# Performance work log

Hardware: AMD Instinct MI355X
Metric: run time of the kernel (lower is better)

The kernel has to match this reference:

```python
import jax, jax.numpy as jnp
import numpy as np

B_, L, DM = 2, 2048, 1024
DI, N, K, R = 2048, 16, 4, 64  # d_inner, d_state, d_conv, dt_rank


def setup_inputs() -> dict:
    key = jax.random.key(0)
    ks = jax.random.split(key, 8)
    return {
        "x": jax.random.normal(ks[0], (B_, L, DM), jnp.float32),
        "W_in": jax.random.normal(ks[1], (DM, 2 * DI), jnp.float32) * 0.02,
        "w_conv": jax.random.normal(ks[2], (DI, K), jnp.float32) * 0.1,
        "b_conv": jnp.zeros((DI,), jnp.float32),
        "W_x": jax.random.normal(ks[3], (DI, R + 2 * N), jnp.float32) * 0.02,
        "W_dt": jax.random.normal(ks[4], (R, DI), jnp.float32) * 0.02,
        "b_dt": jnp.full((DI,), -4.6, jnp.float32),  # softplus(b_dt) ~ 0.01 dt init
        "A_log": jnp.log(jnp.broadcast_to(jnp.arange(1, N + 1, dtype=jnp.float32), (DI, N))),
        "D": jnp.ones((DI,), jnp.float32),
        "W_out": jax.random.normal(ks[5], (DI, DM), jnp.float32) * 0.02,
        "gamma": jnp.ones((DM,), jnp.float32),
        "beta": jnp.zeros((DM,), jnp.float32),
    }


def reference(x, W_in, w_conv, b_conv, W_x, W_dt, b_dt, A_log, D, W_out, gamma, beta):
    Bb, Ll, Dm = x.shape
    Di, Kk = w_conv.shape
    Nn = A_log.shape[1]
    Rr = W_dt.shape[0]
    # in_proj -> (u, z)
    xz = x @ W_in  # [B,L,2*Di]
    u, z = jnp.split(xz, 2, axis=-1)
    # depthwise causal conv1d (kernel K, left pad K-1) + SiLU
    up = jnp.pad(u, ((0, 0), (Kk - 1, 0), (0, 0)))
    conv = b_conv + sum(up[:, k:k + Ll, :] * w_conv[:, k] for k in range(Kk))
    u = jax.nn.silu(conv)  # [B,L,Di]
    # x_proj -> dt, B, C
    dbc = u @ W_x
    dt, Bm, Cm = dbc[..., :Rr], dbc[..., Rr:Rr + Nn], dbc[..., Rr + Nn:]
    delta = jax.nn.softplus(dt @ W_dt + b_dt)  # [B,L,Di]
    A = -jnp.exp(A_log)  # [Di,N]

    def step(h, inputs):
        d_t, B_t, C_t, u_t = inputs  # [B,Di],[B,N],[B,N],[B,Di]
        dA = jnp.exp(d_t[..., None] * A)            # [B,Di,N]
        h = h * dA + (d_t * u_t)[..., None] * B_t[:, None, :]
        y = jnp.einsum('bdn,bn->bd', h, C_t)
        return h, y

    h0 = jnp.zeros((Bb, Di, Nn), x.dtype)
    _, ys = jax.lax.scan(step, h0, (delta.transpose(1, 0, 2), Bm.transpose(1, 0, 2),
                                    Cm.transpose(1, 0, 2), u.transpose(1, 0, 2)))
    y = ys.transpose(1, 0, 2)        # [B,L,Di]
    y = y + u * D                    # skip term
    y = y * jax.nn.silu(z)           # gate
    out = y @ W_out                  # [B,L,Dm]
    # LayerNorm
    mu = out.mean(-1, keepdims=True)
    var = ((out - mu) ** 2).mean(-1, keepdims=True)
    out = (out - mu) * jax.lax.rsqrt(var + 1e-5) * gamma + beta
    # dropout p=0 -> identity; residual
    return out + x
```

## Files before the change

### kernel.cpp

```cpp
#include <hip/hip_runtime.h>
#include <math.h>

#define L_SEQ 2048
#define DMOD  1024
#define DIN   2048
#define NBATCH 2
#define NTOK  (NBATCH * L_SEQ)
#define NST   16
#define RRANK 64
#define LOG2E 1.44269504088896f

#define GCHUNK 128
#define CLEN   (L_SEQ / GCHUNK)
#define SCHUNK 8
#define NSTAGE (CLEN / SCHUNK)

#define G4_KS   4
#define G4_KC   (2048 / G4_KS)
#define G2_KS   16
#define G2_KC   (2048 / G2_KS)

typedef __attribute__((ext_vector_type(8))) short  short8;
typedef __attribute__((ext_vector_type(4))) float  f32x4;

__device__ __forceinline__ ushort f2bf(float f) {
    unsigned u = __float_as_uint(f);
    u += 0x7fffu + ((u >> 16) & 1u);
    return (ushort)(u >> 16);
}
__device__ __forceinline__ float bf2f(ushort u) {
    return __uint_as_float(((unsigned)u) << 16);
}
__device__ __forceinline__ float fexp2(float x) {
    return __builtin_amdgcn_exp2f(x);
}

__device__ __forceinline__ void gload16(const ushort* g, ushort* l) {
    __builtin_amdgcn_global_load_lds(
        (const __attribute__((address_space(1))) unsigned int*)g,
        (__attribute__((address_space(3))) unsigned int*)l,
        16, 0, 0);
}

__device__ __forceinline__ void cast_body(
    const float* __restrict__ src, ushort* __restrict__ dst, int bid, int tid)
{
    int i = (bid * 256 + tid) * 8;
    float4 a = *(const float4*)(src + i);
    float4 b = *(const float4*)(src + i + 4);
    ushort4 o0 = make_ushort4(f2bf(a.x), f2bf(a.y), f2bf(a.z), f2bf(a.w));
    ushort4 o1 = make_ushort4(f2bf(b.x), f2bf(b.y), f2bf(b.z), f2bf(b.w));
    *(ushort4*)(dst + i)     = o0;
    *(ushort4*)(dst + i + 4) = o1;
}

__device__ __forceinline__ void tcast_body(
    const float* __restrict__ src, ushort* __restrict__ dst,
    int R, int C, int bx, int by, int tid)
{
    __shared__ float t[32][33];
    int tx = tid & 31;
    int ty = tid >> 5;
    int c0 = bx * 32;
    int r0 = by * 32;
    #pragma unroll
    for (int i = 0; i < 4; ++i)
        t[ty + i * 8][tx] = src[(size_t)(r0 + ty + i * 8) * C + c0 + tx];
    __syncthreads();
    #pragma unroll
    for (int i = 0; i < 4; ++i)
        dst[(size_t)(c0 + ty + i * 8) * R + r0 + tx] = f2bf(t[tx][ty + i * 8]);
}

__global__ __launch_bounds__(256) void prep_k(
    const float* __restrict__ x, const float* __restrict__ W_in,
    const float* __restrict__ W_dt, const float* __restrict__ W_x,
    const float* __restrict__ W_out,
    ushort* __restrict__ xb, ushort* __restrict__ Wib,
    ushort* __restrict__ Wdtb, ushort* __restrict__ Wxb,
    ushort* __restrict__ Wob)
{
    int bid = blockIdx.x, tid = threadIdx.x;
    if (bid < 2048) {
        cast_body(x, xb, bid, tid);
    } else if (bid < 6144) {
        int t = bid - 2048;
        tcast_body(W_in, Wib, 1024, 4096, t & 127, t >> 7, tid);
    } else if (bid < 6272) {
        int t = bid - 6144;
        tcast_body(W_dt, Wdtb, 64, 2048, t & 63, t >> 6, tid);
    } else if (bid < 6464) {
        int t = bid - 6272;
        tcast_body(W_x, Wxb, 2048, 96, t % 3, t / 3, tid);
    } else {
        int t = bid - 6464;
        tcast_body(W_out, Wob, 2048, 1024, t & 31, t >> 5, tid);
    }
}

__global__ __launch_bounds__(512, 2) void gemm8p(
    const ushort* __restrict__ A,
    const ushort* __restrict__ Bt,
    ushort* __restrict__ C,
    int K, int kslice, int ldc, size_t zstride,
    ushort* __restrict__ C2, int nsplit)
{
    __shared__ ushort lds[65536];

    const int tid  = threadIdx.x;
    const int wave = tid >> 6;
    const int lane = tid & 63;
    const int wr   = wave >> 2;
    const int wc   = wave & 3;

    const int gx = gridDim.x;
    int flat = blockIdx.y * gx + blockIdx.x;
    const int cpx = (gx * gridDim.y) >> 3;
    flat = (flat & 7) * cpx + (flat >> 3);
    const int bx = flat % gx;
    const int by = flat / gx;
    const int m0 = by * 256;
    const int n0 = bx * 256;
    const int kbeg = blockIdx.z * kslice;
    const int NT   = kslice >> 6;

    const int rr  = tid >> 2;
    const int gsw = ((tid & 3) ^ ((tid >> 3) & 3)) * 8;
    const ushort* a0 = A  + (size_t)(m0 + rr)        * K + kbeg + gsw;
    const ushort* a1 = A  + (size_t)(m0 + 128 + rr)  * K + kbeg + gsw;
    const ushort* b0 = Bt + (size_t)(n0 + rr)        * K + kbeg + gsw;
    const ushort* b1 = Bt + (size_t)(n0 + 128 + rr)  * K + kbeg + gsw;

    #define STAGE_U(op_, ks_, kt_, bf_) do {                                   \
        const int ko_ = (kt_) * 64 + (ks_) * 32;                               \
        ushort* l_ = lds + (bf_) * 32768 + (op_) * 16384 + (ks_) * 8192        \
                         + wave * 512;                                         \
        if ((op_) == 0) { gload16(a0 + ko_, l_); gload16(a1 + ko_, l_ + 4096); }\
        else            { gload16(b0 + ko_, l_); gload16(b1 + ko_, l_ + 4096); }\
    } while (0)

    const int lr  = lane & 15;
    const int swr = ((lane >> 4) ^ ((lr >> 1) & 3)) * 8;

    #define LDA(i_, ks_) (*(const short8*)&lds[buf * 32768 + (ks_) * 8192      \
        + (wr * 128 + (i_) * 16 + lr) * 32 + swr])
    #define LDB(j_, ks_) (*(const short8*)&lds[buf * 32768 + 16384             \
        + (ks_) * 8192 + (wc * 64 + (j_) * 16 + lr) * 32 + swr])

    f32x4 acc[8][4];
    #pragma unroll
    for (int i = 0; i < 8; ++i)
        #pragma unroll
        for (int j = 0; j < 4; ++j)
            acc[i][j] = (f32x4){0.f, 0.f, 0.f, 0.f};

    STAGE_U(0, 0, 0, 0); STAGE_U(1, 0, 0, 0);
    STAGE_U(0, 1, 0, 0); STAGE_U(1, 1, 0, 0);
    asm volatile("s_waitcnt vmcnt(4)" ::: "memory");
    __builtin_amdgcn_s_barrier();

    short8 a_[4], b_[4];

    for (int t = 0; t < NT; ++t) {
        const int buf = t & 1, nb = buf ^ 1;
        const bool st = (t + 1 < NT);

        #pragma unroll
        for (int i = 0; i < 4; ++i) a_[i] = LDA(i, 0);
        #pragma unroll
        for (int j = 0; j < 4; ++j) b_[j] = LDB(j, 0);
        if (st) STAGE_U(0, 0, t + 1, nb);
        __builtin_amdgcn_s_barrier();
        asm volatile("s_waitcnt lgkmcnt(0)" ::: "memory");
        __builtin_amdgcn_sched_barrier(0);
        __builtin_amdgcn_s_setprio(1);
        #pragma unroll
        for (int i = 0; i < 4; ++i)
            #pragma unroll
            for (int j = 0; j < 4; ++j)
                acc[i][j] = __builtin_amdgcn_mfma_f32_16x16x32_bf16(
                    a_[i], b_[j], acc[i][j], 0, 0, 0);
        __builtin_amdgcn_s_setprio(0);
        __builtin_amdgcn_s_barrier();

        #pragma unroll
        for (int i = 0; i < 4; ++i) a_[i] = LDA(4 + i, 0);
        if (st) {
            STAGE_U(1, 0, t + 1, nb);
            asm volatile("s_waitcnt vmcnt(4)" ::: "memory");
        } else {
            asm volatile("s_waitcnt vmcnt(0)" ::: "memory");
        }
        __builtin_amdgcn_s_barrier();
        asm volatile("s_waitcnt lgkmcnt(0)" ::: "memory");
        __builtin_amdgcn_sched_barrier(0);
        __builtin_amdgcn_s_setprio(1);
        #pragma unroll
        for (int i = 0; i < 4; ++i)
            #pragma unroll
            for (int j = 0; j < 4; ++j)
                acc[4 + i][j] = __builtin_amdgcn_mfma_f32_16x16x32_bf16(
                    a_[i], b_[j], acc[4 + i][j], 0, 0, 0);
        __builtin_amdgcn_s_setprio(0);
        __builtin_amdgcn_s_barrier();

        #pragma unroll
        for (int i = 0; i < 4; ++i) a_[i] = LDA(i, 1);
        #pragma unroll
        for (int j = 0; j < 4; ++j) b_[j] = LDB(j, 1);
        if (st) STAGE_U(0, 1, t + 1, nb);
        __builtin_amdgcn_s_barrier();
        asm volatile("s_waitcnt lgkmcnt(0)" ::: "memory");
        __builtin_amdgcn_sched_barrier(0);
        __builtin_amdgcn_s_setprio(1);
        #pragma unroll
        for (int i = 0; i < 4; ++i)
            #pragma unroll
            for (int j = 0; j < 4; ++j)
                acc[i][j] = __builtin_amdgcn_mfma_f32_16x16x32_bf16(
                    a_[i], b_[j], acc[i][j], 0, 0, 0);
        __builtin_amdgcn_s_setprio(0);
        __builtin_amdgcn_s_barrier();

        #pragma unroll
        for (int i = 0; i < 4; ++i) a_[i] = LDA(4 + i, 1);
        if (st) {
            STAGE_U(1, 1, t + 1, nb);
            asm volatile("s_waitcnt vmcnt(4)" ::: "memory");
        }
        __builtin_amdgcn_s_barrier();
        asm volatile("s_waitcnt lgkmcnt(0)" ::: "memory");
        __builtin_amdgcn_sched_barrier(0);
        __builtin_amdgcn_s_setprio(1);
        #pragma unroll
        for (int i = 0; i < 4; ++i)
            #pragma unroll
            for (int j = 0; j < 4; ++j)
                acc[4 + i][j] = __builtin_amdgcn_mfma_f32_16x16x32_bf16(
                    a_[i], b_[j], acc[4 + i][j], 0, 0, 0);
        __builtin_amdgcn_s_setprio(0);
        __builtin_amdgcn_s_barrier();
    }
    #undef STAGE_U
    #undef LDA
    #undef LDB

    ushort* Cp = C + (size_t)blockIdx.z * zstride;
    int ncol = n0;
    if (C2 != nullptr && n0 >= nsplit) { Cp = C2; ncol = n0 - nsplit; }
    const int rb = m0 + wr * 128 + ((lane >> 4) << 2);
    const int cb = ncol + wc * 64 + lr;
    #pragma unroll
    for (int i = 0; i < 8; ++i)
        #pragma unroll
        for (int j = 0; j < 4; ++j)
            #pragma unroll
            for (int r = 0; r < 4; ++r)
                Cp[(size_t)(rb + i * 16 + r) * ldc + cb + j * 16] =
                    f2bf(acc[i][j][r]);
}

template<int EPI, int OBF>
__global__ __launch_bounds__(256) void gemm_mfma(
    const ushort* __restrict__ A,
    const ushort* __restrict__ Bt,
    void* __restrict__ Cv,
    int M, int N, int K, int ldc, const float* __restrict__ bias)
{
    __shared__ ushort As[128 * 32];
    __shared__ ushort Bs[128 * 32];

    const int tid  = threadIdx.x;
    const int wave = tid >> 6;
    const int lane = tid & 63;
    const int wm   = (wave & 1) * 64;
    const int wn   = (wave >> 1) * 64;
    const int m0   = blockIdx.y * 128;
    const int n0   = blockIdx.x * 128;

    const int srow = lane >> 2;
    const int sg   = (lane & 3) ^ ((srow >> 1) & 3);
    const ushort* gA0 = A  + (size_t)(m0 + wave * 32 + srow)      * K + sg * 8;
    const ushort* gA1 = A  + (size_t)(m0 + wave * 32 + 16 + srow) * K + sg * 8;
    const ushort* gB0 = Bt + (size_t)(n0 + wave * 32 + srow)      * K + sg * 8;
    const ushort* gB1 = Bt + (size_t)(n0 + wave * 32 + 16 + srow) * K + sg * 8;
    ushort* lA0 = As + (wave * 32)      * 32;
    ushort* lA1 = As + (wave * 32 + 16) * 32;
    ushort* lB0 = Bs + (wave * 32)      * 32;
    ushort* lB1 = Bs + (wave * 32 + 16) * 32;

    const int lrow = lane & 15;
    const int swr  = ((lane >> 4) ^ ((lrow >> 1) & 3)) * 8;

    f32x4 acc[4][4];
    #pragma unroll
    for (int i = 0; i < 4; ++i)
        #pragma unroll
        for (int j = 0; j < 4; ++j)
            acc[i][j] = (f32x4){0.f, 0.f, 0.f, 0.f};

    for (int k0 = 0; k0 < K; k0 += 32) {
        __syncthreads();
        gload16(gA0 + k0, lA0);
        gload16(gA1 + k0, lA1);
        gload16(gB0 + k0, lB0);
        gload16(gB1 + k0, lB1);
        __syncthreads();

        short8 af[4], bfr[4];
        #pragma unroll
        for (int i = 0; i < 4; ++i) {
            af[i]  = *(const short8*)&As[(wm + i * 16 + lrow) * 32 + swr];
            bfr[i] = *(const short8*)&Bs[(wn + i * 16 + lrow) * 32 + swr];
        }
        #pragma unroll
        for (int i = 0; i < 4; ++i)
            #pragma unroll
            for (int j = 0; j < 4; ++j)
                acc[i][j] = __builtin_amdgcn_mfma_f32_16x16x32_bf16(
                    af[i], bfr[j], acc[i][j], 0, 0, 0);
    }

    const int rb = m0 + wm + ((lane >> 4) << 2);
    const int cb = n0 + wn + lrow;

    float bias4[4];
    if (EPI == 1) {
        #pragma unroll
        for (int j = 0; j < 4; ++j) bias4[j] = bias[cb + j * 16];
    }

    #pragma unroll
    for (int i = 0; i < 4; ++i)
        #pragma unroll
        for (int j = 0; j < 4; ++j)
            #pragma unroll
            for (int r = 0; r < 4; ++r) {
                float v = acc[i][j][r];
                int col = cb + j * 16;
                if (EPI == 1) {
                    v += bias4[j];
                    if (v <= 20.f) {
                        float t = fexp2(v * LOG2E);
                        v = __builtin_amdgcn_logf(1.f + t) * (1.f / LOG2E);
                    }
                }
                size_t off = (size_t)(rb + i * 16 + r) * ldc + col;
                if (OBF) ((ushort*)Cv)[off] = f2bf(v);
                else     ((float*)Cv)[off]  = v;
            }
}

__global__ __launch_bounds__(256) void gemm2_mfma(
    const ushort* __restrict__ A,
    const ushort* __restrict__ Bt,
    float* __restrict__ part)
{
    __shared__ ushort As[128 * 32];
    __shared__ ushort Bs[128 * 32];

    const int K = 2048;
    const int tid  = threadIdx.x;
    const int wave = tid >> 6;
    const int lane = tid & 63;
    const int wm   = (wave & 1) * 64;
    const int wn   = (wave >> 1) * 64;
    const int m0   = blockIdx.x * 128;
    const int ks   = blockIdx.z;

    const int srow = lane >> 2;
    const int sg   = (lane & 3) ^ ((srow >> 1) & 3);
    int rB0 = wave * 32 + srow;      if (rB0 > 95) rB0 = 95;
    int rB1 = wave * 32 + 16 + srow; if (rB1 > 95) rB1 = 95;
    const ushort* gA0 = A  + (size_t)(m0 + wave * 32 + srow)      * K + sg * 8;
    const ushort* gA1 = A  + (size_t)(m0 + wave * 32 + 16 + srow) * K + sg * 8;
    const ushort* gB0 = Bt + (size_t)rB0 * K + sg * 8;
    const ushort* gB1 = Bt + (size_t)rB1 * K + sg * 8;
    ushort* lA0 = As + (wave * 32)      * 32;
    ushort* lA1 = As + (wave * 32 + 16) * 32;
    ushort* lB0 = Bs + (wave * 32)      * 32;
    ushort* lB1 = Bs + (wave * 32 + 16) * 32;

    const int lrow = lane & 15;
    const int swr  = ((lane >> 4) ^ ((lrow >> 1) & 3)) * 8;

    f32x4 acc[4][4];
    #pragma unroll
    for (int i = 0; i < 4; ++i)
        #pragma unroll
        for (int j = 0; j < 4; ++j)
            acc[i][j] = (f32x4){0.f, 0.f, 0.f, 0.f};

    const int kbeg = ks * G2_KC, kend = kbeg + G2_KC;
    for (int k0 = kbeg; k0 < kend; k0 += 32) {
        __syncthreads();
        gload16(gA0 + k0, lA0);
        gload16(gA1 + k0, lA1);
        gload16(gB0 + k0, lB0);
        gload16(gB1 + k0, lB1);
        __syncthreads();

        short8 af[4], bfr[4];
        #pragma unroll
        for (int i = 0; i < 4; ++i) {
            af[i]  = *(const short8*)&As[(wm + i * 16 + lrow) * 32 + swr];
            bfr[i] = *(const short8*)&Bs[(wn + i * 16 + lrow) * 32 + swr];
        }
        #pragma unroll
        for (int i = 0; i < 4; ++i)
            #pragma unroll
            for (int j = 0; j < 4; ++j)
                acc[i][j] = __builtin_amdgcn_mfma_f32_16x16x32_bf16(
                    af[i], bfr[j], acc[i][j], 0, 0, 0);
    }

    float* po = part + (size_t)ks * NTOK * 96;
    const int rb = m0 + wm + ((lane >> 4) << 2);
    const int cb = wn + lrow;
    #pragma unroll
    for (int i = 0; i < 4; ++i)
        #pragma unroll
        for (int j = 0; j < 4; ++j) {
            int col = cb + j * 16;
            if (col < 96) {
                #pragma unroll
                for (int r = 0; r < 4; ++r)
                    po[(size_t)(rb + i * 16 + r) * 96 + col] = acc[i][j][r];
            }
        }
}

__global__ __launch_bounds__(256) void gemm2_reduce_dt(
    const float* __restrict__ part, float* __restrict__ dbc,
    ushort* __restrict__ dtb)
{
    int i = (blockIdx.x * 256 + threadIdx.x) * 4;
    float4 s = *(const float4*)(part + i);
    #pragma unroll
    for (int ks = 1; ks < G2_KS; ++ks) {
        float4 v = *(const float4*)(part + (size_t)ks * NTOK * 96 + i);
        s.x += v.x; s.y += v.y; s.z += v.z; s.w += v.w;
    }
    *(float4*)(dbc + i) = s;
    int col = i % 96;
    if (col < RRANK) {
        int row = i / 96;
        ushort* q = dtb + (size_t)row * RRANK + col;
        q[0] = f2bf(s.x); q[1] = f2bf(s.y); q[2] = f2bf(s.z); q[3] = f2bf(s.w);
    }
}

__global__ __launch_bounds__(256) void conv_silu_k(
    const ushort* __restrict__ up, const float* __restrict__ w_conv,
    const float* __restrict__ b_conv, ushort* __restrict__ ub)
{
    const int token = blockIdx.x;
    const int d     = threadIdx.x * 8;
    const int t     = token & (L_SEQ - 1);

    float4 w[8];
    const float4* pw = (const float4*)(w_conv + (size_t)d * 4);
    #pragma unroll
    for (int i = 0; i < 8; ++i) w[i] = pw[i];

    float acc[8];
    {
        float4 bc0 = *(const float4*)(b_conv + d);
        float4 bc1 = *(const float4*)(b_conv + d + 4);
        acc[0] = bc0.x; acc[1] = bc0.y; acc[2] = bc0.z; acc[3] = bc0.w;
        acc[4] = bc1.x; acc[5] = bc1.y; acc[6] = bc1.z; acc[7] = bc1.w;
    }

    #pragma unroll
    for (int k = 0; k < 4; ++k) {
        int tt = t - 3 + k;
        if (tt >= 0) {
            short8 v = *(const short8*)(up + (size_t)(token - 3 + k) * 2048 + d);
            #pragma unroll
            for (int i = 0; i < 8; ++i)
                acc[i] += bf2f((ushort)v[i]) * (&w[i].x)[k];
        }
    }

    short8 o;
    #pragma unroll
    for (int i = 0; i < 8; ++i) {
        float s = acc[i] / (1.f + __expf(-acc[i]));
        o[i] = (short)f2bf(s);
    }
    *(short8*)(ub + (size_t)token * DIN + d) = o;
}

__global__ __launch_bounds__(256) void scan_part1(
    const float* __restrict__ dlt,
    const ushort* __restrict__ ub,
    const float* __restrict__ dbc,
    const float* __restrict__ A_log,
    float* __restrict__ c_out,
    float* __restrict__ dsum_out)
{
    int chunk = blockIdx.x & (GCHUNK - 1);
    int dg    = (blockIdx.x >> 7) & 7;
    int b     = blockIdx.x >> 10;
    int wave  = threadIdx.x >> 6;
    int lane  = threadIdx.x & 63;
    int d     = dg * 256 + wave * 64 + lane;

    __shared__ float sB[4][SCHUNK][16];

    float Al[NST];
    const float4* pA = (const float4*)(A_log + (size_t)d * NST);
    #pragma unroll
    for (int q = 0; q < 4; ++q) {
        float4 a = pA[q];
        Al[q*4+0] = -__expf(a.x) * LOG2E;
        Al[q*4+1] = -__expf(a.y) * LOG2E;
        Al[q*4+2] = -__expf(a.z) * LOG2E;
        Al[q*4+3] = -__expf(a.w) * LOG2E;
    }

    float h[NST];
    #pragma unroll
    for (int n = 0; n < NST; ++n) h[n] = 0.f;
    float dsum = 0.f;

    const size_t tokbase = (size_t)b * L_SEQ + (size_t)chunk * CLEN;
    const float*  pD = dlt + tokbase * 2048 + d;
    const ushort* pU = ub  + tokbase * 2048 + d;
    const float*  pB = dbc + tokbase * 96 + RRANK;

    float rd[2][SCHUNK], ru[2][SCHUNK], rb[2][2];

    #pragma unroll
    for (int i = 0; i < SCHUNK; ++i) {
        rd[0][i] = pD[(size_t)i * 2048];
        ru[0][i] = bf2f(pU[(size_t)i * 2048]);
    }
    #pragma unroll
    for (int i = 0; i < 2; ++i) {
        int e = i * 64 + lane;
        rb[0][i] = pB[(size_t)(e >> 4) * 96 + (e & 15)];
    }

    #pragma unroll
    for (int st = 0; st < NSTAGE; ++st) {
        const int cur = st & 1, nxt = cur ^ 1;
        #pragma unroll
        for (int i = 0; i < 2; ++i) {
            int e = i * 64 + lane;
            sB[wave][e >> 4][e & 15] = rb[cur][i];
        }
        if (st + 1 < NSTAGE) {
            const size_t to = (size_t)(st + 1) * SCHUNK;
            #pragma unroll
            for (int i = 0; i < SCHUNK; ++i) {
                rd[nxt][i] = pD[(to + i) * 2048];
                ru[nxt][i] = bf2f(pU[(to + i) * 2048]);
            }
            #pragma unroll
            for (int i = 0; i < 2; ++i) {
                int e = i * 64 + lane;
                rb[nxt][i] = pB[(to + (e >> 4)) * 96 + (e & 15)];
            }
        }
        #pragma unroll
        for (int s = 0; s < SCHUNK; ++s) {
            float delta = rd[cur][s];
            float du    = delta * ru[cur][s];
            dsum += delta;
            #pragma unroll
            for (int q = 0; q < 4; ++q) {
                float4 bq = *(const float4*)&sB[wave][s][q * 4];
                h[q*4+0] = h[q*4+0] * fexp2(delta * Al[q*4+0]) + du * bq.x;
                h[q*4+1] = h[q*4+1] * fexp2(delta * Al[q*4+1]) + du * bq.y;
                h[q*4+2] = h[q*4+2] * fexp2(delta * Al[q*4+2]) + du * bq.z;
                h[q*4+3] = h[q*4+3] * fexp2(delta * Al[q*4+3]) + du * bq.w;
            }
        }
    }

    size_t base = (((size_t)b * DIN + d) * GCHUNK + chunk) * NST;
    #pragma unroll
    for (int q = 0; q < 4; ++q)
        *(float4*)&c_out[base + q * 4] = make_float4(h[q*4], h[q*4+1], h[q*4+2], h[q*4+3]);
    dsum_out[((size_t)b * DIN + d) * GCHUNK + chunk] = dsum;
}

__global__ __launch_bounds__(256) void scan_part2(
    float* __restrict__ cbuf,
    const float* __restrict__ dsum_in,
    const float* __restrict__ A_log)
{
    int idx = blockIdx.x * 256 + threadIdx.x;
    int n   = idx & 15;
    int d   = (idx >> 4) & (DIN - 1);
    int b   = idx >> 15;

    float Al = -__expf(A_log[(size_t)d * NST + n]) * LOG2E;
    size_t cb = ((size_t)b * DIN + d) * GCHUNK;

    float h = 0.f;
    for (int ch = 0; ch < GCHUNK; ++ch) {
        size_t o = (cb + ch) * NST + n;
        float c  = cbuf[o];
        float dA = fexp2(Al * dsum_in[cb + ch]);
        cbuf[o]  = h;
        h = h * dA + c;
    }
}

__global__ __launch_bounds__(256) void scan_part3(
    const float* __restrict__ dlt,
    const ushort* __restrict__ zb,
    ushort* __restrict__ ub,
    const float* __restrict__ dbc,
    const float* __restrict__ A_log,
    const float* __restrict__ Dp,
    const float* __restrict__ h_start)
{
    int chunk = blockIdx.x & (GCHUNK - 1);
    int dg    = (blockIdx.x >> 7) & 7;
    int b     = blockIdx.x >> 10;
    int wave  = threadIdx.x >> 6;
    int lane  = threadIdx.x & 63;
    int d     = dg * 256 + wave * 64 + lane;

    __shared__ float sBC[4][SCHUNK][32];

    float Al[NST];
    const float4* pA = (const float4*)(A_log + (size_t)d * NST);
    #pragma unroll
    for (int q = 0; q < 4; ++q) {
        float4 a = pA[q];
        Al[q*4+0] = -__expf(a.x) * LOG2E;
        Al[q*4+1] = -__expf(a.y) * LOG2E;
        Al[q*4+2] = -__expf(a.z) * LOG2E;
        Al[q*4+3] = -__expf(a.w) * LOG2E;
    }
    float Dd = Dp[d];

    float h[NST];
    size_t hb = (((size_t)b * DIN + d) * GCHUNK + chunk) * NST;
    #pragma unroll
    for (int q = 0; q < 4; ++q) {
        float4 v = *(const float4*)&h_start[hb + q * 4];
        h[q*4] = v.x; h[q*4+1] = v.y; h[q*4+2] = v.z; h[q*4+3] = v.w;
    }

    const size_t tokbase = (size_t)b * L_SEQ + (size_t)chunk * CLEN;
    const float*  pD = dlt + tokbase * 2048 + d;
    const ushort* pZ = zb  + tokbase * 2048 + d;
    ushort*       pU = ub  + tokbase * 2048 + d;
    const float*  pB = dbc + tokbase * 96 + RRANK;

    float rd[2][SCHUNK], ru[2][SCHUNK], rz[2][SCHUNK], rb[2][4];

    #pragma unroll
    for (int i = 0; i < SCHUNK; ++i) {
        rd[0][i] = pD[(size_t)i * 2048];
        ru[0][i] = bf2f(pU[(size_t)i * 2048]);
        rz[0][i] = bf2f(pZ[(size_t)i * 2048]);
    }
    #pragma unroll
    for (int i = 0; i < 4; ++i) {
        int e = i * 64 + lane;
        rb[0][i] = pB[(size_t)(e >> 5) * 96 + (e & 31)];
    }

    #pragma unroll
    for (int st = 0; st < NSTAGE; ++st) {
        const int cur = st & 1, nxt = cur ^ 1;
        #pragma unroll
        for (int i = 0; i < 4; ++i) {
            int e = i * 64 + lane;
            sBC[wave][e >> 5][e & 31] = rb[cur][i];
        }
        if (st + 1 < NSTAGE) {
            const size_t to = (size_t)(st + 1) * SCHUNK;
            #pragma unroll
            for (int i = 0; i < SCHUNK; ++i) {
                rd[nxt][i] = pD[(to + i) * 2048];
                ru[nxt][i] = bf2f(pU[(to + i) * 2048]);
                rz[nxt][i] = bf2f(pZ[(to + i) * 2048]);
            }
            #pragma unroll
            for (int i = 0; i < 4; ++i) {
                int e = i * 64 + lane;
                rb[nxt][i] = pB[(to + (e >> 5)) * 96 + (e & 31)];
            }
        }
        #pragma unroll
        for (int s = 0; s < SCHUNK; ++s) {
            float delta = rd[cur][s];
            float u     = ru[cur][s];
            float du    = delta * u;
            float y = 0.f;
            #pragma unroll
            for (int q = 0; q < 4; ++q) {
                float4 bq = *(const float4*)&sBC[wave][s][q * 4];
                float4 cq = *(const float4*)&sBC[wave][s][16 + q * 4];
                h[q*4+0] = h[q*4+0] * fexp2(delta * Al[q*4+0]) + du * bq.x; y += h[q*4+0] * cq.x;
                h[q*4+1] = h[q*4+1] * fexp2(delta * Al[q*4+1]) + du * bq.y; y += h[q*4+1] * cq.y;
                h[q*4+2] = h[q*4+2] * fexp2(delta * Al[q*4+2]) + du * bq.z; y += h[q*4+2] * cq.z;
                h[q*4+3] = h[q*4+3] * fexp2(delta * Al[q*4+3]) + du * bq.w; y += h[q*4+3] * cq.w;
            }
            float z  = rz[cur][s];
            float sz = z / (1.f + __expf(-z));
            pU[((size_t)st * SCHUNK + s) * 2048] = f2bf((y + u * Dd) * sz);
        }
    }
}

__global__ __launch_bounds__(256) void ln4_k(
    const ushort* __restrict__ part,
    const float* __restrict__ x,
    const float* __restrict__ gamma, const float* __restrict__ beta,
    float* __restrict__ out)
{
    int row = blockIdx.x;
    int tid = threadIdx.x;
    const size_t off = (size_t)row * DMOD + tid * 4;

    float4 v = {0.f, 0.f, 0.f, 0.f};
    #pragma unroll
    for (int ks = 0; ks < G4_KS; ++ks) {
        ushort4 p = *(const ushort4*)(part + (size_t)ks * NTOK * DMOD + off);
        v.x += bf2f(p.x); v.y += bf2f(p.y); v.z += bf2f(p.z); v.w += bf2f(p.w);
    }

    float s  = v.x + v.y + v.z + v.w;
    float s2 = v.x * v.x + v.y * v.y + v.z * v.z + v.w * v.w;
    #pragma unroll
    for (int off2 = 32; off2 > 0; off2 >>= 1) {
        s  += __shfl_down(s, off2);
        s2 += __shfl_down(s2, off2);
    }
    __shared__ float ws[4], ws2[4];
    int wave = tid >> 6, lane = tid & 63;
    if (lane == 0) { ws[wave] = s; ws2[wave] = s2; }
    __syncthreads();
    if (tid == 0) {
        float ts = 0.f, ts2 = 0.f;
        #pragma unroll
        for (int w = 0; w < 4; ++w) { ts += ws[w]; ts2 += ws2[w]; }
        ws[0] = ts; ws2[0] = ts2;
    }
    __syncthreads();
    float mu  = ws[0] * (1.f / DMOD);
    float var = ws2[0] * (1.f / DMOD) - mu * mu;
    float rs  = rsqrtf(var + 1e-5f);

    float4 g  = ((const float4*)gamma)[tid];
    float4 be = ((const float4*)beta)[tid];
    float4 xr = *(const float4*)(x + off);
    float4 o;
    o.x = (v.x - mu) * rs * g.x + be.x + xr.x;
    o.y = (v.y - mu) * rs * g.y + be.y + xr.y;
    o.z = (v.z - mu) * rs * g.z + be.z + xr.z;
    o.w = (v.w - mu) * rs * g.w + be.w + xr.w;
    *(float4*)(out + off) = o;
}

extern "C" void kernel_launch(void* const* d_in, const int* in_sizes, int n_in,
                              void* d_out, int out_size, void* d_ws, size_t ws_size,
                              hipStream_t stream)
{
    const float* x      = (const float*)d_in[0];
    const float* W_in   = (const float*)d_in[1];
    const float* w_conv = (const float*)d_in[2];
    const float* b_conv = (const float*)d_in[3];
    const float* W_x    = (const float*)d_in[4];
    const float* W_dt   = (const float*)d_in[5];
    const float* b_dt   = (const float*)d_in[6];
    const float* A_log  = (const float*)d_in[7];
    const float* Dp     = (const float*)d_in[8];
    const float* W_out  = (const float*)d_in[9];
    const float* gamma  = (const float*)d_in[10];
    const float* beta   = (const float*)d_in[11];
    float* out = (float*)d_out;

    char* ws = (char*)d_ws;
    const size_t MB = 1024 * 1024;
    ushort* zb     = (ushort*)(ws);
    ushort* ub     = (ushort*)(ws + 16 * MB);
    float*  dlt    = (float*)(ws + 32 * MB);
    float*  dbc    = (float*)(ws + 64 * MB);
    ushort* Wdtb   = (ushort*)(ws + 65 * MB + 512 * 1024);
    ushort* Wxb    = (ushort*)(ws + 65 * MB + 768 * 1024);
    ushort* dtb    = (ushort*)(ws + 66 * MB + 128 * 1024);
    float*  dsum   = (float*)(ws + 67 * MB);
    ushort* Wob    = (ushort*)(ws + 69 * MB);
    float*  c_buf  = (float*)(ws + 73 * MB);
    ushort* xb     = (ushort*)(ws + 73 * MB);
    ushort* Wib    = (ushort*)(ws + 81 * MB);
    ushort* ub_pre = (ushort*)(ws + 89 * MB);
    float*  g2part = (float*)(ws + 73 * MB);
    ushort* g4part = (ushort*)(ws + 32 * MB);

    dim3 blk(256);

    prep_k<<<dim3(8512), blk, 0, stream>>>(x, W_in, W_dt, W_x, W_out,
                                           xb, Wib, Wdtb, Wxb, Wob);
    gemm8p<<<dim3(16, 16, 1), dim3(512), 0, stream>>>(
        xb, Wib, ub_pre, 1024, 1024, 2048, 0, zb, 2048);
    conv_silu_k<<<dim3(NTOK), blk, 0, stream>>>(ub_pre, w_conv, b_conv, ub);
    gemm2_mfma<<<dim3(32, 1, G2_KS), blk, 0, stream>>>(ub, Wxb, g2part);
    gemm2_reduce_dt<<<dim3(NTOK * 96 / 4 / 256), blk, 0, stream>>>(g2part, dbc, dtb);
    gemm_mfma<1, 0><<<dim3(16, 32), blk, 0, stream>>>(
        dtb, Wdtb, dlt, 4096, 2048, 64, 2048, b_dt);
    scan_part1<<<dim3(NBATCH * 8 * GCHUNK), blk, 0, stream>>>(
        dlt, ub, dbc, A_log, c_buf, dsum);
    scan_part2<<<dim3(NBATCH * DIN * NST / 256), blk, 0, stream>>>(
        c_buf, dsum, A_log);
    scan_part3<<<dim3(NBATCH * 8 * GCHUNK), blk, 0, stream>>>(
        dlt, zb, ub, dbc, A_log, Dp, c_buf);
    gemm8p<<<dim3(4, 16, G4_KS), dim3(512), 0, stream>>>(
        ub, Wob, g4part, 2048, G4_KC, DMOD, (size_t)NTOK * DMOD,
        nullptr, 0x7fffffff);
    ln4_k<<<dim3(NTOK), blk, 0, stream>>>(g4part, x, gamma, beta, out);
}
```

Before: 314.4 us.

## Restructure 256x256 GEMM into four-stage ring of 32-wide K halves

Replaces the double-buffered 64-wide K tile pipeline with a 4-slot LDS ring of 32-wide K slices, prefetching three slices ahead instead of one. The intent is to hide more global load latency behind MFMA work, with finer-grained vmcnt waits tuned to how many loads are still outstanding. It keeps the same LDS footprint but adds more complex wait logic at the pipeline tail. It also risks races if the prefetch overwrites a slot another wave is still reading.

```diff
diff --git a/kernel.cpp b/kernel.cpp
--- a/kernel.cpp
+++ b/kernel.cpp
@@ -122,7 +122,7 @@
     const int m0 = by * 256;
     const int n0 = bx * 256;
     const int kbeg = blockIdx.z * kslice;
-    const int NT   = kslice >> 6;
+    const int NH   = kslice >> 5;
 
     const int rr  = tid >> 2;
     const int gsw = ((tid & 3) ^ ((tid >> 3) & 3)) * 8;
@@ -131,10 +131,9 @@
     const ushort* b0 = Bt + (size_t)(n0 + rr)        * K + kbeg + gsw;
     const ushort* b1 = Bt + (size_t)(n0 + 128 + rr)  * K + kbeg + gsw;
 
-    #define STAGE_U(op_, ks_, kt_, bf_) do {                                   \
-        const int ko_ = (kt_) * 64 + (ks_) * 32;                               \
-        ushort* l_ = lds + (bf_) * 32768 + (op_) * 16384 + (ks_) * 8192        \
-                         + wave * 512;                                         \
+    #define STAGE_H(op_, h_) do {                                              \
+        const int ko_ = (h_) * 32;                                             \
+        ushort* l_ = lds + ((h_) & 3) * 16384 + (op_) * 8192 + wave * 512;     \
         if ((op_) == 0) { gload16(a0 + ko_, l_); gload16(a1 + ko_, l_ + 4096); }\
         else            { gload16(b0 + ko_, l_); gload16(b1 + ko_, l_ + 4096); }\
     } while (0)
@@ -142,10 +141,10 @@
     const int lr  = lane & 15;
     const int swr = ((lane >> 4) ^ ((lr >> 1) & 3)) * 8;
 
-    #define LDA(i_, ks_) (*(const short8*)&lds[buf * 32768 + (ks_) * 8192      \
+    #define LDAH(i_, h_) (*(const short8*)&lds[((h_) & 3) * 16384              \
         + (wr * 128 + (i_) * 16 + lr) * 32 + swr])
-    #define LDB(j_, ks_) (*(const short8*)&lds[buf * 32768 + 16384             \
-        + (ks_) * 8192 + (wc * 64 + (j_) * 16 + lr) * 32 + swr])
+    #define LDBH(j_, h_) (*(const short8*)&lds[((h_) & 3) * 16384 + 8192       \
+        + (wc * 64 + (j_) * 16 + lr) * 32 + swr])
 
     f32x4 acc[8][4];
     #pragma unroll
@@ -154,22 +153,22 @@
         for (int j = 0; j < 4; ++j)
             acc[i][j] = (f32x4){0.f, 0.f, 0.f, 0.f};
 
-    STAGE_U(0, 0, 0, 0); STAGE_U(1, 0, 0, 0);
-    STAGE_U(0, 1, 0, 0); STAGE_U(1, 1, 0, 0);
-    asm volatile("s_waitcnt vmcnt(4)" ::: "memory");
+    STAGE_H(0, 0); STAGE_H(1, 0);
+    STAGE_H(0, 1); STAGE_H(1, 1);
+    STAGE_H(0, 2); STAGE_H(1, 2);
+    asm volatile("s_waitcnt vmcnt(8)" ::: "memory");
     __builtin_amdgcn_s_barrier();
 
     short8 a_[4], b_[4];
 
-    for (int t = 0; t < NT; ++t) {
-        const int buf = t & 1, nb = buf ^ 1;
-        const bool st = (t + 1 < NT);
-
-        #pragma unroll
-        for (int i = 0; i < 4; ++i) a_[i] = LDA(i, 0);
-        #pragma unroll
-        for (int j = 0; j < 4; ++j) b_[j] = LDB(j, 0);
-        if (st) STAGE_U(0, 0, t + 1, nb);
+    for (int h = 0; h < NH; ++h) {
+        const bool st = (h + 3 < NH);
+
+        #pragma unroll
+        for (int i = 0; i < 4; ++i) a_[i] = LDAH(i, h);
+        #pragma unroll
+        for (int j = 0; j < 4; ++j) b_[j] = LDBH(j, h);
+        if (st) STAGE_H(0, h + 3);
         __builtin_amdgcn_s_barrier();
         asm volatile("s_waitcnt lgkmcnt(0)" ::: "memory");
         __builtin_amdgcn_sched_barrier(0);
@@ -184,13 +183,14 @@
         __builtin_amdgcn_s_barrier();
 
         #pragma unroll
-        for (int i = 0; i < 4; ++i) a_[i] = LDA(4 + i, 0);
-        if (st) {
-            STAGE_U(1, 0, t + 1, nb);
+        for (int i = 0; i < 4; ++i) a_[i] = LDAH(4 + i, h);
+        if (st) STAGE_H(1, h + 3);
+        if (h + 4 <= NH - 1)
+            asm volatile("s_waitcnt vmcnt(8)" ::: "memory");
+        else if (h + 3 == NH - 1)
             asm volatile("s_waitcnt vmcnt(4)" ::: "memory");
-        } else {
+        else
             asm volatile("s_waitcnt vmcnt(0)" ::: "memory");
-        }
         __builtin_amdgcn_s_barrier();
         asm volatile("s_waitcnt lgkmcnt(0)" ::: "memory");
         __builtin_amdgcn_sched_barrier(0);
@@ -203,47 +203,10 @@
                     a_[i], b_[j], acc[4 + i][j], 0, 0, 0);
         __builtin_amdgcn_s_setprio(0);
         __builtin_amdgcn_s_barrier();
-
-        #pragma unroll
-        for (int i = 0; i < 4; ++i) a_[i] = LDA(i, 1);
-        #pragma unroll
-        for (int j = 0; j < 4; ++j) b_[j] = LDB(j, 1);
-        if (st) STAGE_U(0, 1, t + 1, nb);
-        __builtin_amdgcn_s_barrier();
-        asm volatile("s_waitcnt lgkmcnt(0)" ::: "memory");
-        __builtin_amdgcn_sched_barrier(0);
-        __builtin_amdgcn_s_setprio(1);
-        #pragma unroll
-        for (int i = 0; i < 4; ++i)
-            #pragma unroll
-            for (int j = 0; j < 4; ++j)
-                acc[i][j] = __builtin_amdgcn_mfma_f32_16x16x32_bf16(
-                    a_[i], b_[j], acc[i][j], 0, 0, 0);
-        __builtin_amdgcn_s_setprio(0);
-        __builtin_amdgcn_s_barrier();
-
-        #pragma unroll
-        for (int i = 0; i < 4; ++i) a_[i] = LDA(4 + i, 1);
-        if (st) {
-            STAGE_U(1, 1, t + 1, nb);
-            asm volatile("s_waitcnt vmcnt(4)" ::: "memory");
-        }
-        __builtin_amdgcn_s_barrier();
-        asm volatile("s_waitcnt lgkmcnt(0)" ::: "memory");
-        __builtin_amdgcn_sched_barrier(0);
-        __builtin_amdgcn_s_setprio(1);
-        #pragma unroll
-        for (int i = 0; i < 4; ++i)
-            #pragma unroll
-            for (int j = 0; j < 4; ++j)
-                acc[4 + i][j] = __builtin_amdgcn_mfma_f32_16x16x32_bf16(
-                    a_[i], b_[j], acc[4 + i][j], 0, 0, 0);
-        __builtin_amdgcn_s_setprio(0);
-        __builtin_amdgcn_s_barrier();
-    }
-    #undef STAGE_U
-    #undef LDA
-    #undef LDB
+    }
+    #undef STAGE_H
+    #undef LDAH
+    #undef LDBH
 
     ushort* Cp = C + (size_t)blockIdx.z * zstride;
     int ncol = n0;
```

Measured after the change: 319.2 us. Within noise of the previous version (+1.5%).
